# Performance work log

Measured on AMD Instinct MI355X. Metric: run time of the kernel, lower is better.

Reference implementation:

```python
import jax, jax.numpy as jnp
import numpy as np

IMG_H, IMG_W = 168, 300
VOCAB = 300
MAX_EP = 30
GRU_H = 256
INST_LEN = 18


def _conv(x, w, b, stride):
    y = jax.lax.conv_general_dilated(x, w, (stride, stride), 'VALID',
                                     dimension_numbers=('NCHW', 'OIHW', 'NCHW'))
    return y + b[None, :, None, None]


def setup_inputs() -> dict:
    key = jax.random.key(0)
    k = jax.random.split(key, 20)
    n = lambda i, shape, s=0.05: jax.random.normal(k[i], shape, jnp.float32) * s
    return {
        'x': jax.random.normal(k[0], (1, 3, IMG_H, IMG_W), jnp.float32),
        'input_inst': jax.random.randint(k[1], (1, INST_LEN), 0, VOCAB),
        'tx': jax.random.randint(k[2], (1,), 0, MAX_EP + 1),
        'hx': n(3, (1, 256), 1.0),
        'cx': n(4, (1, 256), 1.0),
        'conv1_w': n(5, (128, 3, 8, 8)), 'conv1_b': jnp.zeros((128,), jnp.float32),
        'conv2_w': n(6, (64, 128, 4, 4)), 'conv2_b': jnp.zeros((64,), jnp.float32),
        'conv3_w': n(7, (64, 64, 4, 4)), 'conv3_b': jnp.zeros((64,), jnp.float32),
        'emb': n(8, (VOCAB, 32), 1.0),
        'gru_wih': n(9, (3 * GRU_H, 32)), 'gru_whh': n(10, (3 * GRU_H, GRU_H)),
        'gru_bih': jnp.zeros((3 * GRU_H,), jnp.float32),
        'gru_bhh': jnp.zeros((3 * GRU_H,), jnp.float32),
        'attn_w': n(11, (5, 64, GRU_H)), 'attn_b': jnp.zeros((5, 64), jnp.float32),
        'time_emb': n(12, (MAX_EP + 1, 32), 1.0),
        'lin_w': n(13, (256, 5 * 8 * 17)), 'lin_b': jnp.zeros((256,), jnp.float32),
        'lstm_wih': n(14, (1024, 256)), 'lstm_whh': n(15, (1024, 256)),
        'lstm_bih': jnp.zeros((1024,), jnp.float32),
        'lstm_bhh': jnp.zeros((1024,), jnp.float32),
        'critic_w': n(16, (1, 256 + 32)), 'critic_b': jnp.zeros((1,), jnp.float32),
        'actor_w': n(17, (3, 256 + 32)), 'actor_b': jnp.zeros((3,), jnp.float32),
    }


def reference(x, input_inst, tx, hx, cx,
              conv1_w, conv1_b, conv2_w, conv2_b, conv3_w, conv3_b,
              emb, gru_wih, gru_whh, gru_bih, gru_bhh,
              attn_w, attn_b, time_emb, lin_w, lin_b,
              lstm_wih, lstm_whh, lstm_bih, lstm_bhh,
              critic_w, critic_b, actor_w, actor_b):
    # --- image backbone ---
    h1 = jax.nn.relu(_conv(x, conv1_w, conv1_b, 4))          # [1,128,41,74]
    h2 = jax.nn.relu(_conv(h1, conv2_w, conv2_b, 2))         # [1,64,19,36]
    img = jax.nn.relu(_conv(h2, conv3_w, conv3_b, 2))        # [1,64,8,17]

    # --- GRU instruction encoder (per-token loop -> scan) ---
    words = emb[input_inst[0]]                               # [L,32]

    def gru_step(h, w_t):
        gi = gru_wih @ w_t + gru_bih                         # [768]
        gh = gru_whh @ h + gru_bhh
        ir, iz, ig = jnp.split(gi, 3)
        hr, hz, hg = jnp.split(gh, 3)
        r = jax.nn.sigmoid(ir + hr)
        z = jax.nn.sigmoid(iz + hz)
        g = jnp.tanh(ig + r * hg)
        return (1.0 - z) * g + z * h, None

    instr, _ = jax.lax.scan(gru_step, jnp.zeros((GRU_H,), x.dtype), words)  # [256]

    # --- 5-branch gated attention (1x1 convs == channel contraction) ---
    attn = jax.nn.relu(jnp.einsum('koc,c->ko', attn_w, instr) + attn_b)     # [5,64]
    attn_vecs = jnp.einsum('kc,bchw->bkhw', attn, img)       # [1,5,8,17]

    feat = jax.nn.relu(attn_vecs.reshape(1, -1) @ lin_w.T + lin_b)          # [1,256]

    # --- LSTMCell ---
    gates = feat @ lstm_wih.T + lstm_bih + hx @ lstm_whh.T + lstm_bhh       # [1,1024]
    i, f, g, o = jnp.split(gates, 4, axis=1)
    c2 = jax.nn.sigmoid(f) * cx + jax.nn.sigmoid(i) * jnp.tanh(g)
    h2x = jax.nn.sigmoid(o) * jnp.tanh(c2)

    feat2 = jnp.concatenate([h2x, time_emb[tx]], axis=1)     # [1,288]
    critic = feat2 @ critic_w.T + critic_b                   # [1,1]
    actor = feat2 @ actor_w.T + actor_b                      # [1,3]
    return critic, actor, h2x, c2
```

## Files before the change

kernel.cpp:

```cpp
#include <hip/hip_runtime.h>
#include <math.h>

#define MAGIC 0x3C96A5F1
#define NGRU 8
#define NWRK 240
#define NBLK (NGRU + NWRK)
#define WSTR 260
#define ATAG 7u
#define FTAG 9u
#define LTAG 11u

__device__ __forceinline__ float sigmf(float x) { return 1.0f / (1.0f + expf(-x)); }

__device__ __forceinline__ void st_agent(float* p, float v) {
    __hip_atomic_store(p, v, __ATOMIC_RELAXED, __HIP_MEMORY_SCOPE_AGENT);
}
__device__ __forceinline__ void st_flag(int* p) {
    __hip_atomic_store(p, MAGIC, __ATOMIC_RELEASE, __HIP_MEMORY_SCOPE_AGENT);
}
__device__ __forceinline__ void poll_flags(const int* f, int n, int tid) {
    if (tid < n) {
        while (__hip_atomic_load(f + tid, __ATOMIC_RELAXED, __HIP_MEMORY_SCOPE_AGENT) != MAGIC) {}
    }
    __builtin_amdgcn_fence(__ATOMIC_ACQUIRE, "agent");
    __syncthreads();
}
__device__ __forceinline__ void st_pk(unsigned long long* p, unsigned tag, float v) {
    __hip_atomic_store(p, ((unsigned long long)tag << 32) | (unsigned long long)__float_as_uint(v),
                       __ATOMIC_RELAXED, __HIP_MEMORY_SCOPE_AGENT);
}
__device__ __forceinline__ float poll_pk(const unsigned long long* p, unsigned tag) {
    unsigned long long v;
    do { v = __hip_atomic_load(p, __ATOMIC_RELAXED, __HIP_MEMORY_SCOPE_AGENT); }
    while ((unsigned)(v >> 32) != tag);
    return __uint_as_float((unsigned)(v & 0xffffffffu));
}

__global__ __launch_bounds__(256) void mega_k(
    const float* __restrict__ x, const int* __restrict__ inst, const int* __restrict__ tx,
    const float* __restrict__ hx, const float* __restrict__ cx,
    const float* __restrict__ conv1_w, const float* __restrict__ conv1_b,
    const float* __restrict__ conv2_w, const float* __restrict__ conv2_b,
    const float* __restrict__ conv3_w, const float* __restrict__ conv3_b,
    const float* __restrict__ emb,
    const float* __restrict__ wih, const float* __restrict__ whh,
    const float* __restrict__ bih, const float* __restrict__ bhh,
    const float* __restrict__ attn_w, const float* __restrict__ attn_b,
    const float* __restrict__ time_emb,
    const float* __restrict__ lin_w, const float* __restrict__ lin_b,
    const float* __restrict__ lstm_wih, const float* __restrict__ lstm_whh,
    const float* __restrict__ lstm_bih, const float* __restrict__ lstm_bhh,
    const float* __restrict__ critic_w, const float* __restrict__ critic_b,
    const float* __restrict__ actor_w, const float* __restrict__ actor_b,
    float* __restrict__ c1o, float* __restrict__ c2o, float* __restrict__ img,
    unsigned long long* __restrict__ hpk,
    unsigned long long* __restrict__ apk,
    unsigned long long* __restrict__ fpk,
    unsigned long long* __restrict__ lpk,
    int* __restrict__ flags,
    float* __restrict__ out) {

    int* c1f  = flags;
    int* c2f  = flags + 240;
    int* imgf = flags + 480;

    __shared__ float whh_s[96 * WSTR];
    __shared__ float gi_s[18 * 96];
    __shared__ float wt_all[18 * 32];
    __shared__ float bhh_s[96];
    __shared__ __align__(16) float h_s[256];
    __shared__ __align__(16) float attn_s[320];
    __shared__ __align__(16) float av_s[680];
    __shared__ __align__(16) float f2_s[288];
    __shared__ __align__(16) float ws[2048];
    __shared__ __align__(16) float feat_ls[256];

    const int tid = threadIdx.x;
    const int b = blockIdx.x;

    if (b < NGRU) {
        const int d = tid >> 3;
        const int ch = tid & 7;
        const int dimg = b * 32 + d;

        for (int i = tid; i < 96 * 64; i += 256) {
            int lr = i >> 6, q = i & 63;
            int gr = (lr >> 5) * 256 + b * 32 + (lr & 31);
            float4 v = *reinterpret_cast<const float4*>(whh + gr * 256 + q * 4);
            *reinterpret_cast<float4*>(&whh_s[lr * WSTR + q * 4]) = v;
        }
        for (int i = tid; i < 18 * 32; i += 256) wt_all[i] = emb[inst[i >> 5] * 32 + (i & 31)];
        if (tid < 96) bhh_s[tid] = bhh[(tid >> 5) * 256 + b * 32 + (tid & 31)];
        h_s[tid] = 0.0f;
        __syncthreads();

        for (int u = tid; u < 18 * 96; u += 256) {
            int t = u / 96, r = u % 96;
            int R = (r >> 5) * 256 + b * 32 + (r & 31);
            const float4* w4 = reinterpret_cast<const float4*>(wih + R * 32);
            const float4* e4 = reinterpret_cast<const float4*>(wt_all + t * 32);
            float s = 0.f;
            #pragma unroll
            for (int q = 0; q < 8; q++) {
                float4 a = w4[q], c = e4[q];
                s += a.x * c.x + a.y * c.y + a.z * c.z + a.w * c.w;
            }
            gi_s[u] = s + bih[R];
        }
        __syncthreads();

        for (int t = 0; t < 18; t++) {
            const float4* hr4 = reinterpret_cast<const float4*>(h_s + ch * 32);
            const float4* w0 = reinterpret_cast<const float4*>(&whh_s[d * WSTR + ch * 32]);
            const float4* w1 = reinterpret_cast<const float4*>(&whh_s[(32 + d) * WSTR + ch * 32]);
            const float4* w2 = reinterpret_cast<const float4*>(&whh_s[(64 + d) * WSTR + ch * 32]);
            float p0 = 0.f, p1 = 0.f, p2 = 0.f;
            #pragma unroll
            for (int j = 0; j < 8; j++) {
                float4 c = hr4[j];
                float4 a0 = w0[j], a1 = w1[j], a2 = w2[j];
                p0 += a0.x * c.x + a0.y * c.y + a0.z * c.z + a0.w * c.w;
                p1 += a1.x * c.x + a1.y * c.y + a1.z * c.z + a1.w * c.w;
                p2 += a2.x * c.x + a2.y * c.y + a2.z * c.z + a2.w * c.w;
            }
            p0 += __shfl_xor(p0, 1); p0 += __shfl_xor(p0, 2); p0 += __shfl_xor(p0, 4);
            p1 += __shfl_xor(p1, 1); p1 += __shfl_xor(p1, 2); p1 += __shfl_xor(p1, 4);
            p2 += __shfl_xor(p2, 1); p2 += __shfl_xor(p2, 2); p2 += __shfl_xor(p2, 4);
            if (ch == 0) {
                float ghr = p0 + bhh_s[d];
                float ghz = p1 + bhh_s[32 + d];
                float ghg = p2 + bhh_s[64 + d];
                float rr = sigmf(gi_s[t * 96 + d] + ghr);
                float zz = sigmf(gi_s[t * 96 + 32 + d] + ghz);
                float gg = tanhf(gi_s[t * 96 + 64 + d] + rr * ghg);
                float hn = (1.f - zz) * gg + zz * h_s[dimg];
                st_pk(hpk + t * 256 + dimg, (unsigned)(t + 1), hn);
            }
            float hv = poll_pk(hpk + t * 256 + tid, (unsigned)(t + 1));
            __syncthreads();
            h_s[tid] = hv;
            __syncthreads();
        }

        {
            int lr = tid >> 2, ln = tid & 3;
            if (lr < 40) {
                int a = b * 40 + lr;
                const float4* w4 = reinterpret_cast<const float4*>(attn_w + a * 256 + ln * 64);
                const float4* h4 = reinterpret_cast<const float4*>(h_s + ln * 64);
                float s = 0.f;
                #pragma unroll
                for (int q = 0; q < 16; q++) {
                    float4 aa = w4[q], cc = h4[q];
                    s += aa.x * cc.x + aa.y * cc.y + aa.z * cc.z + aa.w * cc.w;
                }
                s += __shfl_xor(s, 1); s += __shfl_xor(s, 2);
                if (ln == 0) st_pk(apk + a, ATAG, fmaxf(s + attn_b[a], 0.f));
            }
        }
        attn_s[tid] = poll_pk(apk + tid, ATAG);
        if (tid < 64) attn_s[256 + tid] = poll_pk(apk + 256 + tid, ATAG);
        if (tid < 64) {
            while (__hip_atomic_load(imgf + tid, __ATOMIC_RELAXED, __HIP_MEMORY_SCOPE_AGENT) != MAGIC) {}
        }
        __builtin_amdgcn_fence(__ATOMIC_ACQUIRE, "agent");
        __syncthreads();

        for (int o = tid; o < 680; o += 256) {
            int k = o / 136, rem = o - k * 136;
            const float* ag = attn_s + k * 64;
            const float* ip = img + rem;
            float s = 0.f;
            #pragma unroll 8
            for (int c = 0; c < 64; c++) s = fmaf(ag[c], ip[c * 136], s);
            av_s[o] = s;
        }
        __syncthreads();

        {
            int lr = tid >> 3, ln = tid & 7;
            int fr = b * 32 + lr;
            const float4* w4 = reinterpret_cast<const float4*>(lin_w + fr * 680);
            const float4* a4 = reinterpret_cast<const float4*>(av_s);
            float s = 0.f;
            for (int c = ln; c < 170; c += 8) {
                float4 a = w4[c], cc = a4[c];
                s += a.x * cc.x + a.y * cc.y + a.z * cc.z + a.w * cc.w;
            }
            s += __shfl_xor(s, 1); s += __shfl_xor(s, 2); s += __shfl_xor(s, 4);
            if (ln == 0) st_pk(fpk + fr, FTAG, fmaxf(s + lin_b[fr], 0.f));
        }

        if (b == 0) {
            float ig = poll_pk(lpk + tid, LTAG);
            float fg = poll_pk(lpk + 256 + tid, LTAG);
            float gg = poll_pk(lpk + 512 + tid, LTAG);
            float og = poll_pk(lpk + 768 + tid, LTAG);
            float cc = sigmf(fg) * cx[tid] + sigmf(ig) * tanhf(gg);
            float hh = sigmf(og) * tanhf(cc);
            out[260 + tid] = cc;
            out[4 + tid] = hh;
            f2_s[tid] = hh;
            if (tid < 32) f2_s[256 + tid] = time_emb[tx[0] * 32 + tid];
            __syncthreads();
            int wv = tid >> 6, ln = tid & 63;
            const float* wr = (wv == 0) ? critic_w : (actor_w + (wv - 1) * 288);
            float p = 0.f;
            for (int i = ln; i < 288; i += 64) p = fmaf(f2_s[i], wr[i], p);
            #pragma unroll
            for (int off = 32; off >= 1; off >>= 1) p += __shfl_down(p, off);
            if (ln == 0) out[wv] = p + ((wv == 0) ? critic_b[0] : actor_b[wv - 1]);
            __syncthreads();
            for (int i = tid; i < 544; i += 256) flags[i] = 0;
            for (int i = tid; i < 18 * 256; i += 256) hpk[i] = 0ull;
            for (int i = tid; i < 320; i += 256) apk[i] = 0ull;
            if (tid < 256) fpk[tid] = 0ull;
            for (int i = tid; i < 1024; i += 256) lpk[i] = 0ull;
        }
    } else {
        const int wb = b - NGRU;

        for (int tile = wb; tile < 1536; tile += NWRK) {
            int co = tile / 12, chunk = tile % 12;
            __syncthreads();
            if (tid < 192) ws[tid] = conv1_w[co * 192 + tid];
            __syncthreads();
            int pix = chunk * 256 + tid;
            if (pix < 3034) {
                int oh = pix / 74, ow = pix % 74;
                const float* xp = x + oh * 4 * 300 + ow * 4;
                float acc = conv1_b[co];
                #pragma unroll
                for (int ci = 0; ci < 3; ci++) {
                    #pragma unroll
                    for (int kh = 0; kh < 8; kh++) {
                        const float* row = xp + ci * (168 * 300) + kh * 300;
                        const float* wr = ws + ci * 64 + kh * 8;
                        float4 q0 = *reinterpret_cast<const float4*>(row);
                        float4 q1 = *reinterpret_cast<const float4*>(row + 4);
                        acc += q0.x * wr[0] + q0.y * wr[1] + q0.z * wr[2] + q0.w * wr[3]
                             + q1.x * wr[4] + q1.y * wr[5] + q1.z * wr[6] + q1.w * wr[7];
                    }
                }
                st_agent(c1o + co * 3034 + pix, fmaxf(acc, 0.f));
            }
        }
        __syncthreads();
        if (tid == 0) st_flag(c1f + wb);
        poll_flags(c1f, NWRK, tid);

        for (int tile = wb; tile < 192; tile += NWRK) {
            int co = tile / 3, chunk = tile % 3;
            __syncthreads();
            for (int i = tid; i < 2048; i += 256) ws[i] = conv2_w[co * 2048 + i];
            __syncthreads();
            int pix = chunk * 256 + tid;
            if (pix < 684) {
                int oh = pix / 36, ow = pix % 36;
                const float* base = c1o + oh * 2 * 74 + ow * 2;
                float acc = conv2_b[co];
                #pragma unroll 4
                for (int ci = 0; ci < 128; ci++) {
                    const float* ip = base + ci * 3034;
                    const float* wc = ws + ci * 16;
                    #pragma unroll
                    for (int kh = 0; kh < 4; kh++) {
                        const float* row = ip + kh * 74;
                        const float* wr = wc + kh * 4;
                        float2 a0 = *reinterpret_cast<const float2*>(row);
                        float2 a1 = *reinterpret_cast<const float2*>(row + 2);
                        acc += a0.x * wr[0] + a0.y * wr[1] + a1.x * wr[2] + a1.y * wr[3];
                    }
                }
                st_agent(c2o + co * 684 + pix, fmaxf(acc, 0.f));
            }
        }
        __syncthreads();
        if (tid == 0) st_flag(c2f + wb);

        if (wb < 64) {
            poll_flags(c2f, NWRK, tid);
            {
                int co = wb;
                for (int i = tid; i < 1024; i += 256) ws[i] = conv3_w[co * 1024 + i];
                __syncthreads();
                if (tid < 136) {
                    int oh = tid / 17, ow = tid % 17;
                    const float* base = c2o + oh * 2 * 36 + ow * 2;
                    float acc = conv3_b[co];
                    #pragma unroll 4
                    for (int ci = 0; ci < 64; ci++) {
                        const float* ip = base + ci * 684;
                        const float* wc = ws + ci * 16;
                        #pragma unroll
                        for (int kh = 0; kh < 4; kh++) {
                            const float* row = ip + kh * 36;
                            const float* wr = wc + kh * 4;
                            float2 a0 = *reinterpret_cast<const float2*>(row);
                            float2 a1 = *reinterpret_cast<const float2*>(row + 2);
                            acc += a0.x * wr[0] + a0.y * wr[1] + a1.x * wr[2] + a1.y * wr[3];
                        }
                    }
                    st_agent(img + co * 136 + tid, fmaxf(acc, 0.f));
                }
                __syncthreads();
                if (tid == 0) st_flag(imgf + wb);
            }
            feat_ls[tid] = poll_pk(fpk + tid, FTAG);
            __syncthreads();
            {
                int lr = tid >> 4, ln = tid & 15;
                int r = wb * 16 + lr;
                const float4* wi4 = reinterpret_cast<const float4*>(lstm_wih + r * 256);
                const float4* wh4 = reinterpret_cast<const float4*>(lstm_whh + r * 256);
                const float4* f4 = reinterpret_cast<const float4*>(feat_ls);
                const float4* x4 = reinterpret_cast<const float4*>(hx);
                float s = 0.f;
                #pragma unroll
                for (int q = 0; q < 4; q++) {
                    float4 a = wi4[ln * 4 + q], c = f4[ln * 4 + q];
                    s += a.x * c.x + a.y * c.y + a.z * c.z + a.w * c.w;
                    float4 dd = wh4[ln * 4 + q], e = x4[ln * 4 + q];
                    s += dd.x * e.x + dd.y * e.y + dd.z * e.z + dd.w * e.w;
                }
                s += __shfl_xor(s, 1); s += __shfl_xor(s, 2);
                s += __shfl_xor(s, 4); s += __shfl_xor(s, 8);
                if (ln == 0) st_pk(lpk + r, LTAG, s + lstm_bih[r] + lstm_bhh[r]);
            }
        }
    }
}

extern "C" void kernel_launch(void* const* d_in, const int* in_sizes, int n_in,
                              void* d_out, int out_size, void* d_ws, size_t ws_size,
                              hipStream_t stream) {
    const float* x        = (const float*)d_in[0];
    const int*   inst     = (const int*)d_in[1];
    const int*   tx       = (const int*)d_in[2];
    const float* hx       = (const float*)d_in[3];
    const float* cx       = (const float*)d_in[4];
    const float* conv1_w  = (const float*)d_in[5];
    const float* conv1_b  = (const float*)d_in[6];
    const float* conv2_w  = (const float*)d_in[7];
    const float* conv2_b  = (const float*)d_in[8];
    const float* conv3_w  = (const float*)d_in[9];
    const float* conv3_b  = (const float*)d_in[10];
    const float* emb      = (const float*)d_in[11];
    const float* gru_wih  = (const float*)d_in[12];
    const float* gru_whh  = (const float*)d_in[13];
    const float* gru_bih  = (const float*)d_in[14];
    const float* gru_bhh  = (const float*)d_in[15];
    const float* attn_w   = (const float*)d_in[16];
    const float* attn_b   = (const float*)d_in[17];
    const float* time_emb = (const float*)d_in[18];
    const float* lin_w    = (const float*)d_in[19];
    const float* lin_b    = (const float*)d_in[20];
    const float* lstm_wih = (const float*)d_in[21];
    const float* lstm_whh = (const float*)d_in[22];
    const float* lstm_bih = (const float*)d_in[23];
    const float* lstm_bhh = (const float*)d_in[24];
    const float* critic_w = (const float*)d_in[25];
    const float* critic_b = (const float*)d_in[26];
    const float* actor_w  = (const float*)d_in[27];
    const float* actor_b  = (const float*)d_in[28];

    float* wsf = (float*)d_ws;
    float* c1o  = wsf;
    float* c2o  = wsf + 388352;
    float* img  = wsf + 432128;
    unsigned long long* hpk = (unsigned long long*)(wsf + 440832);
    unsigned long long* apk = (unsigned long long*)(wsf + 450048);
    unsigned long long* fpk = (unsigned long long*)(wsf + 450688);
    unsigned long long* lpk = (unsigned long long*)(wsf + 451200);
    int* flags = (int*)(wsf + 453248);
    float* out = (float*)d_out;

    mega_k<<<NBLK, 256, 0, stream>>>(x, inst, tx, hx, cx,
                                     conv1_w, conv1_b, conv2_w, conv2_b, conv3_w, conv3_b,
                                     emb, gru_wih, gru_whh, gru_bih, gru_bhh,
                                     attn_w, attn_b, time_emb, lin_w, lin_b,
                                     lstm_wih, lstm_whh, lstm_bih, lstm_bhh,
                                     critic_w, critic_b, actor_w, actor_b,
                                     c1o, c2o, img, hpk, apk, fpk, lpk,
                                     flags, out);
}
```

Measured before the change: 206.4 us.

## Prefetch weights off critical path and add sleep to spin-wait polls

Several ideas are combined here. The GRU blocks warm the cache with their attn_w slice before the recurrence, and they copy their lin_w rows into the idle whh_s shared buffer while waiting for the attention and image flags. The LSTM worker blocks load their lstm weights and compute the hx·whh half before polling for the features, so only the feature dot product remains after the wait. Spin loops on the worker barriers and the feature poll now call s_sleep, which should reduce memory pressure from polling at the cost of slightly higher wake-up latency.

```diff
diff --git a/kernel.cpp b/kernel.cpp
--- a/kernel.cpp
+++ b/kernel.cpp
@@ -18,9 +18,10 @@
 __device__ __forceinline__ void st_flag(int* p) {
     __hip_atomic_store(p, MAGIC, __ATOMIC_RELEASE, __HIP_MEMORY_SCOPE_AGENT);
 }
-__device__ __forceinline__ void poll_flags(const int* f, int n, int tid) {
+__device__ __forceinline__ void poll_flags_s(const int* f, int n, int tid) {
     if (tid < n) {
-        while (__hip_atomic_load(f + tid, __ATOMIC_RELAXED, __HIP_MEMORY_SCOPE_AGENT) != MAGIC) {}
+        while (__hip_atomic_load(f + tid, __ATOMIC_RELAXED, __HIP_MEMORY_SCOPE_AGENT) != MAGIC)
+            __builtin_amdgcn_s_sleep(2);
     }
     __builtin_amdgcn_fence(__ATOMIC_ACQUIRE, "agent");
     __syncthreads();
@@ -33,6 +34,14 @@
     unsigned long long v;
     do { v = __hip_atomic_load(p, __ATOMIC_RELAXED, __HIP_MEMORY_SCOPE_AGENT); }
     while ((unsigned)(v >> 32) != tag);
+    return __uint_as_float((unsigned)(v & 0xffffffffu));
+}
+__device__ __forceinline__ float poll_pk_s(const unsigned long long* p, unsigned tag) {
+    unsigned long long v = __hip_atomic_load(p, __ATOMIC_RELAXED, __HIP_MEMORY_SCOPE_AGENT);
+    while ((unsigned)(v >> 32) != tag) {
+        __builtin_amdgcn_s_sleep(1);
+        v = __hip_atomic_load(p, __ATOMIC_RELAXED, __HIP_MEMORY_SCOPE_AGENT);
+    }
     return __uint_as_float((unsigned)(v & 0xffffffffu));
 }
 
@@ -64,7 +73,7 @@
     int* c2f  = flags + 240;
     int* imgf = flags + 480;
 
-    __shared__ float whh_s[96 * WSTR];
+    __shared__ __align__(16) float whh_s[96 * WSTR];
     __shared__ float gi_s[18 * 96];
     __shared__ float wt_all[18 * 32];
     __shared__ float bhh_s[96];
@@ -93,6 +102,17 @@
         if (tid < 96) bhh_s[tid] = bhh[(tid >> 5) * 256 + b * 32 + (tid & 31)];
         h_s[tid] = 0.0f;
         __syncthreads();
+
+        float wsum = 0.f;
+        {
+            const float4* aw = reinterpret_cast<const float4*>(attn_w + b * 40 * 256);
+            #pragma unroll
+            for (int i = 0; i < 10; i++) {
+                float4 v = aw[tid + i * 256];
+                wsum += v.x + v.y + v.z + v.w;
+            }
+        }
+        asm volatile("" :: "v"(wsum));
 
         for (int u = tid; u < 18 * 96; u += 256) {
             int t = u / 96, r = u % 96;
@@ -158,6 +178,11 @@
                 if (ln == 0) st_pk(apk + a, ATAG, fmaxf(s + attn_b[a], 0.f));
             }
         }
+        {
+            const float4* lw = reinterpret_cast<const float4*>(lin_w + b * 32 * 680);
+            float4* dst = reinterpret_cast<float4*>(whh_s);
+            for (int i = tid; i < 32 * 170; i += 256) dst[i] = lw[i];
+        }
         attn_s[tid] = poll_pk(apk + tid, ATAG);
         if (tid < 64) attn_s[256 + tid] = poll_pk(apk + 256 + tid, ATAG);
         if (tid < 64) {
@@ -180,7 +205,7 @@
         {
             int lr = tid >> 3, ln = tid & 7;
             int fr = b * 32 + lr;
-            const float4* w4 = reinterpret_cast<const float4*>(lin_w + fr * 680);
+            const float4* w4 = reinterpret_cast<const float4*>(whh_s + lr * 680);
             const float4* a4 = reinterpret_cast<const float4*>(av_s);
             float s = 0.f;
             for (int c = ln; c < 170; c += 8) {
@@ -247,7 +272,7 @@
         }
         __syncthreads();
         if (tid == 0) st_flag(c1f + wb);
-        poll_flags(c1f, NWRK, tid);
+        poll_flags_s(c1f, NWRK, tid);
 
         for (int tile = wb; tile < 192; tile += NWRK) {
             int co = tile / 3, chunk = tile % 3;
@@ -279,7 +304,7 @@
         if (tid == 0) st_flag(c2f + wb);
 
         if (wb < 64) {
-            poll_flags(c2f, NWRK, tid);
+            poll_flags_s(c2f, NWRK, tid);
             {
                 int co = wb;
                 for (int i = tid; i < 1024; i += 256) ws[i] = conv3_w[co * 1024 + i];
@@ -306,27 +331,32 @@
                 __syncthreads();
                 if (tid == 0) st_flag(imgf + wb);
             }
-            feat_ls[tid] = poll_pk(fpk + tid, FTAG);
-            __syncthreads();
-            {
-                int lr = tid >> 4, ln = tid & 15;
-                int r = wb * 16 + lr;
-                const float4* wi4 = reinterpret_cast<const float4*>(lstm_wih + r * 256);
-                const float4* wh4 = reinterpret_cast<const float4*>(lstm_whh + r * 256);
-                const float4* f4 = reinterpret_cast<const float4*>(feat_ls);
-                const float4* x4 = reinterpret_cast<const float4*>(hx);
-                float s = 0.f;
-                #pragma unroll
-                for (int q = 0; q < 4; q++) {
-                    float4 a = wi4[ln * 4 + q], c = f4[ln * 4 + q];
-                    s += a.x * c.x + a.y * c.y + a.z * c.z + a.w * c.w;
-                    float4 dd = wh4[ln * 4 + q], e = x4[ln * 4 + q];
-                    s += dd.x * e.x + dd.y * e.y + dd.z * e.z + dd.w * e.w;
-                }
-                s += __shfl_xor(s, 1); s += __shfl_xor(s, 2);
-                s += __shfl_xor(s, 4); s += __shfl_xor(s, 8);
-                if (ln == 0) st_pk(lpk + r, LTAG, s + lstm_bih[r] + lstm_bhh[r]);
-            }
+            int lr = tid >> 4, ln = tid & 15;
+            int r = wb * 16 + lr;
+            const float4* wi4 = reinterpret_cast<const float4*>(lstm_wih + r * 256);
+            const float4* wh4 = reinterpret_cast<const float4*>(lstm_whh + r * 256);
+            const float4* x4 = reinterpret_cast<const float4*>(hx);
+            float4 wi0 = wi4[ln * 4 + 0], wi1 = wi4[ln * 4 + 1];
+            float4 wi2 = wi4[ln * 4 + 2], wi3 = wi4[ln * 4 + 3];
+            float s = 0.f;
+            #pragma unroll
+            for (int q = 0; q < 4; q++) {
+                float4 dd = wh4[ln * 4 + q], e = x4[ln * 4 + q];
+                s += dd.x * e.x + dd.y * e.y + dd.z * e.z + dd.w * e.w;
+            }
+            float bsum = lstm_bih[r] + lstm_bhh[r];
+            feat_ls[tid] = poll_pk_s(fpk + tid, FTAG);
+            __syncthreads();
+            const float4* f4 = reinterpret_cast<const float4*>(feat_ls);
+            float4 c0 = f4[ln * 4 + 0], c1 = f4[ln * 4 + 1];
+            float4 c2 = f4[ln * 4 + 2], c3 = f4[ln * 4 + 3];
+            s += wi0.x * c0.x + wi0.y * c0.y + wi0.z * c0.z + wi0.w * c0.w;
+            s += wi1.x * c1.x + wi1.y * c1.y + wi1.z * c1.z + wi1.w * c1.w;
+            s += wi2.x * c2.x + wi2.y * c2.y + wi2.z * c2.z + wi2.w * c2.w;
+            s += wi3.x * c3.x + wi3.y * c3.y + wi3.z * c3.z + wi3.w * c3.w;
+            s += __shfl_xor(s, 1); s += __shfl_xor(s, 2);
+            s += __shfl_xor(s, 4); s += __shfl_xor(s, 8);
+            if (ln == 0) st_pk(lpk + r, LTAG, s + bsum);
         }
     }
 }
```

After: 201.6 us. -2.3%, faster.
